# Optimization experiments

Measured on AMD Instinct MI355X. Metric: run time of the kernel, lower is better.

## Reference

```python
import jax, jax.numpy as jnp
import numpy as np

D = 512      # d_encoder
H = 8        # num_attn_heads
DH = 64      # d_attn
B = 8
S = 1024


def setup_inputs() -> dict:
    key = jax.random.key(0)
    ks = jax.random.split(key, 12)
    lim_in = 1.0 / np.sqrt(D)
    inp = {
        "Q": jax.random.normal(ks[0], (B, S, D), dtype=jnp.float32),
        "K": jax.random.normal(ks[1], (B, S, D), dtype=jnp.float32),
        "V": jax.random.normal(ks[2], (B, S, D), dtype=jnp.float32),
        # per-head projection weights stacked over heads: [H, D, DH]
        "Wq": jax.random.uniform(ks[3], (H, D, DH), jnp.float32, -lim_in, lim_in),
        "bq": jax.random.uniform(ks[4], (H, DH), jnp.float32, -lim_in, lim_in),
        "Wk": jax.random.uniform(ks[5], (H, D, DH), jnp.float32, -lim_in, lim_in),
        "bk": jax.random.uniform(ks[6], (H, DH), jnp.float32, -lim_in, lim_in),
        "Wv": jax.random.uniform(ks[7], (H, D, DH), jnp.float32, -lim_in, lim_in),
        "bv": jax.random.uniform(ks[8], (H, DH), jnp.float32, -lim_in, lim_in),
        "Wo": jax.random.uniform(ks[9], (D, D), jnp.float32, -lim_in, lim_in),
        "bo": jax.random.uniform(ks[10], (D,), jnp.float32, -lim_in, lim_in),
    }
    return inp


def reference(Q, K, V, Wq, bq, Wk, bk, Wv, bv, Wo, bo):
    scale = 1.0 / np.sqrt(DH).astype(np.float32)
    # per-head projections (the torch loop over heads, batched): [B,H,S,DH]
    Qh = jnp.einsum("bsd,hde->bhse", Q, Wq) + bq[None, :, None, :]
    Kh = jnp.einsum("bsd,hde->bhse", K, Wk) + bk[None, :, None, :]
    Vh = jnp.einsum("bsd,hde->bhse", V, Wv) + bv[None, :, None, :]
    # scaled dot-product attention with materialized scores [B,H,S,S]
    scores = jnp.einsum("bhse,bhte->bhst", Qh, Kh) * scale
    probs = jax.nn.softmax(scores, axis=-1)
    x = jnp.einsum("bhst,bhte->bhse", probs, Vh)  # [B,H,S,DH]
    # NOTE: original torch code does x.view(B, S, H*DH) directly on the
    # (B,H,S,DH) contiguous tensor WITHOUT transposing heads/time; we
    # faithfully replicate that memory-layout reshape.
    x = x.reshape(B, S, H * DH)
    x = x @ Wo + bo
    # dropout p=0.0 (p_drop set to 0 for deterministic reference)
    return x
```

## Files before the change

### kernel.cpp

```cpp
#include <hip/hip_runtime.h>
#include <hip/hip_bf16.h>

#define D_ENC 512
#define NH 8
#define DHD 64
#define BB 8
#define SS 1024

typedef unsigned short u16;
typedef __attribute__((ext_vector_type(8))) short short8;
typedef __attribute__((ext_vector_type(4))) float floatx4;

#define QSCALE 0.18033688011112042f

__device__ inline u16 f2bf(float f) {
    __hip_bfloat16 h = __float2bfloat16(f);
    return *reinterpret_cast<u16*>(&h);
}

__device__ inline void glds16(const u16* g, u16* l) {
    __builtin_amdgcn_global_load_lds(
        (const __attribute__((address_space(1))) void*)g,
        (__attribute__((address_space(3))) void*)l, 16, 0, 0);
}

__global__ __launch_bounds__(256) void prep_all(
    const float* __restrict__ Wq, const float* __restrict__ Wk,
    const float* __restrict__ Wv, const float* __restrict__ Wo,
    const float* __restrict__ Q, const float* __restrict__ K,
    const float* __restrict__ V,
    u16* __restrict__ WqT, u16* __restrict__ WkT, u16* __restrict__ WvT,
    u16* __restrict__ WoT, u16* __restrict__ Xbf)
{
    int bx = blockIdx.x;
    if (bx < 4096) {
        int tid = bx * 256 + threadIdx.x;
        const int WSZ = NH * D_ENC * DHD;
        if (tid < 3 * WSZ) {
            int wi = tid / WSZ, r = tid % WSZ;
            int d = r & 511;
            int e = (r >> 9) & 63;
            int h = r >> 15;
            const float* src = wi == 0 ? Wq : (wi == 1 ? Wk : Wv);
            u16* dst = wi == 0 ? WqT : (wi == 1 ? WkT : WvT);
            dst[r] = f2bf(src[h * (D_ENC * DHD) + d * DHD + e]);
        } else {
            int r = tid - 3 * WSZ;
            int d = r & 511, n = r >> 9;
            WoT[r] = f2bf(Wo[d * D_ENC + n]);
        }
    } else {
        int t = (bx - 4096) * 256 + threadIdx.x;
        int p = t / 524288, i = t % 524288;
        const float* src = p == 0 ? Q : (p == 1 ? K : V);
        const float4* s4 = reinterpret_cast<const float4*>(src) + (size_t)i * 2;
        float4 a = s4[0], b = s4[1];
        u16 hv[8] = { f2bf(a.x), f2bf(a.y), f2bf(a.z), f2bf(a.w),
                      f2bf(b.x), f2bf(b.y), f2bf(b.z), f2bf(b.w) };
        *reinterpret_cast<uint4*>(Xbf + (size_t)t * 8) =
            *reinterpret_cast<const uint4*>(hv);
    }
}

__global__ __launch_bounds__(256, 3) void qkv_gemm(
    const u16* __restrict__ Xbf,
    const u16* __restrict__ WqT, const u16* __restrict__ WkT,
    const u16* __restrict__ WvT,
    const float* __restrict__ bq, const float* __restrict__ bk,
    const float* __restrict__ bv,
    u16* __restrict__ Qh, u16* __restrict__ Kh, u16* __restrict__ VhT)
{
    const int proj = blockIdx.z;
    const u16* X = Xbf + (size_t)proj * (BB * SS * D_ENC);
    const u16* WT = proj == 0 ? WqT : (proj == 1 ? WkT : WvT);
    const float* bias = proj == 0 ? bq : (proj == 1 ? bk : bv);
    u16* out = proj == 0 ? Qh : (proj == 1 ? Kh : VhT);
    const float oscale = proj == 0 ? QSCALE : 1.0f;

    const int m0 = blockIdx.x * 128;
    const int n0 = blockIdx.y * 64;
    __shared__ __align__(16) u16 smem[24576];

    const int tid = threadIdx.x, lane = tid & 63, w = tid >> 6;
    const int q = lane >> 4, l15 = lane & 15;
    const int lr = lane >> 3;
    const int lc = (lane & 7) ^ (lr & 7);

    floatx4 acc[2][4] = {};

    #pragma unroll
    for (int j = 0; j < 4; ++j) {
        int r = (j * 4 + w) * 8 + lr;
        glds16(X + (size_t)(m0 + r) * D_ENC + lc * 8, smem + (j * 4 + w) * 512);
    }
    #pragma unroll
    for (int j = 0; j < 2; ++j) {
        int r = (j * 4 + w) * 8 + lr;
        glds16(WT + (size_t)(n0 + r) * D_ENC + lc * 8,
               smem + 16384 + (j * 4 + w) * 512);
    }

    for (int t = 0; t < 8; ++t) {
        __syncthreads();
        if (t + 1 < 8) {
            const int d1 = (t + 1) * 64;
            u16* ad = smem + ((t + 1) & 1) * 8192;
            u16* bd = smem + 16384 + ((t + 1) & 1) * 4096;
            #pragma unroll
            for (int j = 0; j < 4; ++j) {
                int r = (j * 4 + w) * 8 + lr;
                glds16(X + (size_t)(m0 + r) * D_ENC + d1 + lc * 8,
                       ad + (j * 4 + w) * 512);
            }
            #pragma unroll
            for (int j = 0; j < 2; ++j) {
                int r = (j * 4 + w) * 8 + lr;
                glds16(WT + (size_t)(n0 + r) * D_ENC + d1 + lc * 8,
                       bd + (j * 4 + w) * 512);
            }
        }
        const u16* as_ = smem + (t & 1) * 8192;
        const u16* bs_ = smem + 16384 + (t & 1) * 4096;
        #pragma unroll
        for (int ks = 0; ks < 2; ++ks) {
            const int co = ((ks * 4 + q) ^ (l15 & 7)) * 8;
            short8 a0 = *(const short8*)&as_[(32 * w + l15) * 64 + co];
            short8 a1 = *(const short8*)&as_[(32 * w + 16 + l15) * 64 + co];
            #pragma unroll
            for (int f = 0; f < 4; ++f) {
                short8 bf = *(const short8*)&bs_[(f * 16 + l15) * 64 + co];
                acc[0][f] = __builtin_amdgcn_mfma_f32_16x16x32_bf16(a0, bf, acc[0][f], 0, 0, 0);
                acc[1][f] = __builtin_amdgcn_mfma_f32_16x16x32_bf16(a1, bf, acc[1][f], 0, 0, 0);
            }
        }
    }

    const int b = m0 >> 10, sb = m0 & 1023, h = n0 >> 6;
    if (proj < 2) {
        u16* dst = out + ((size_t)(b * NH + h) * SS + sb) * DHD;
        #pragma unroll
        for (int i = 0; i < 2; ++i)
            #pragma unroll
            for (int f = 0; f < 4; ++f) {
                float bv_ = bias[n0 + f * 16 + l15];
                #pragma unroll
                for (int r = 0; r < 4; ++r)
                    dst[(32 * w + 16 * i + q * 4 + r) * DHD + f * 16 + l15] =
                        f2bf((acc[i][f][r] + bv_) * oscale);
            }
    } else {
        __syncthreads();
        #pragma unroll
        for (int i = 0; i < 2; ++i)
            #pragma unroll
            for (int f = 0; f < 4; ++f) {
                float bv_ = bias[n0 + f * 16 + l15];
                #pragma unroll
                for (int r = 0; r < 4; ++r)
                    smem[(f * 16 + l15) * 136 + 32 * w + 16 * i + q * 4 + r] =
                        f2bf(acc[i][f][r] + bv_);
            }
        __syncthreads();
        u16* dst = out + (size_t)(b * NH + h) * DHD * SS + sb;
        #pragma unroll
        for (int p2 = 0; p2 < 4; ++p2) {
            int c = (tid + 256 * p2) * 8;
            int e = c >> 7, s = c & 127;
            uint4 v = *(const uint4*)&smem[e * 136 + s];
            *(uint4*)&dst[(size_t)e * SS + s] = v;
        }
    }
}

__global__ __launch_bounds__(256, 4) void flash_attn(
    const u16* __restrict__ Qh, const u16* __restrict__ Kh,
    const u16* __restrict__ VhT, u16* __restrict__ Xb)
{
    const int i = blockIdx.x;
    const int s0 = (i >> 6) * 64;
    const size_t bh = (size_t)(((i >> 3) & 7) * 8 + (i & 7));

    __shared__ __align__(16) u16 Ks[2][64 * 64], Vs[2][64 * 64], Ps[64 * 64];

    const int tid = threadIdx.x, lane = tid & 63, w = tid >> 6;
    const int q = lane >> 4, l15 = lane & 15;
    const int lr = lane >> 3, lc = (lane & 7) ^ (lr & 7);

    const u16* qrow = Qh + (bh * SS + s0 + 16 * w + l15) * DHD;
    short8 qb0 = *(const short8*)(qrow + q * 8);
    short8 qb1 = *(const short8*)(qrow + 32 + q * 8);

    const u16* kbase = Kh + bh * SS * DHD;
    const u16* vbase = VhT + bh * DHD * SS;

    #pragma unroll
    for (int j = 0; j < 2; ++j) {
        int r = (j * 4 + w) * 8 + lr;
        glds16(kbase + (size_t)r * DHD + lc * 8, Ks[0] + (j * 4 + w) * 512);
        glds16(vbase + (size_t)r * SS + lc * 8, Vs[0] + (j * 4 + w) * 512);
    }

    floatx4 O[4] = {};
    floatx4 L = {0.f, 0.f, 0.f, 0.f};
    const short8 ones = {16256, 16256, 16256, 16256,
                         16256, 16256, 16256, 16256};

    for (int kt = 0; kt < SS / 64; ++kt) {
        __syncthreads();
        if (kt + 1 < SS / 64) {
            const int k1 = (kt + 1) * 64;
            u16* kd = Ks[(kt + 1) & 1];
            u16* vd = Vs[(kt + 1) & 1];
            #pragma unroll
            for (int j = 0; j < 2; ++j) {
                int r = (j * 4 + w) * 8 + lr;
                glds16(kbase + (size_t)(k1 + r) * DHD + lc * 8,
                       kd + (j * 4 + w) * 512);
                glds16(vbase + (size_t)r * SS + k1 + lc * 8,
                       vd + (j * 4 + w) * 512);
            }
        }
        const u16* ks_ = Ks[kt & 1];
        const u16* vs_ = Vs[kt & 1];

        floatx4 sacc[4] = {};
        #pragma unroll
        for (int f = 0; f < 4; ++f) {
            const int co0 = (q ^ (l15 & 7)) * 8;
            const int co1 = ((4 + q) ^ (l15 & 7)) * 8;
            short8 ka0 = *(const short8*)&ks_[(f * 16 + l15) * 64 + co0];
            short8 ka1 = *(const short8*)&ks_[(f * 16 + l15) * 64 + co1];
            sacc[f] = __builtin_amdgcn_mfma_f32_16x16x32_bf16(ka0, qb0, sacc[f], 0, 0, 0);
            sacc[f] = __builtin_amdgcn_mfma_f32_16x16x32_bf16(ka1, qb1, sacc[f], 0, 0, 0);
        }

        #pragma unroll
        for (int f = 0; f < 4; ++f) {
            ushort4 pk;
            pk.x = f2bf(__builtin_amdgcn_exp2f(sacc[f][0]));
            pk.y = f2bf(__builtin_amdgcn_exp2f(sacc[f][1]));
            pk.z = f2bf(__builtin_amdgcn_exp2f(sacc[f][2]));
            pk.w = f2bf(__builtin_amdgcn_exp2f(sacc[f][3]));
            const int chunk = (2 * f + (q >> 1)) ^ (l15 & 7);
            *(ushort4*)&Ps[(16 * w + l15) * 64 + chunk * 8 + (q & 1) * 4] = pk;
        }

        #pragma unroll
        for (int ks = 0; ks < 2; ++ks) {
            const int co = ((ks * 4 + q) ^ (l15 & 7)) * 8;
            short8 pa = *(const short8*)&Ps[(16 * w + l15) * 64 + co];
            L = __builtin_amdgcn_mfma_f32_16x16x32_bf16(pa, ones, L, 0, 0, 0);
            #pragma unroll
            for (int f = 0; f < 4; ++f) {
                short8 vb = *(const short8*)&vs_[(f * 16 + l15) * 64 + co];
                O[f] = __builtin_amdgcn_mfma_f32_16x16x32_bf16(pa, vb, O[f], 0, 0, 0);
            }
        }
    }

    u16* dst = Xb + (bh * SS + s0) * DHD;
    #pragma unroll
    for (int f = 0; f < 4; ++f)
        #pragma unroll
        for (int r = 0; r < 4; ++r)
            dst[(16 * w + q * 4 + r) * DHD + f * 16 + l15] =
                f2bf(O[f][r] / L[r]);
}

__global__ __launch_bounds__(256, 3) void out_gemm(
    const u16* __restrict__ X, const u16* __restrict__ WT,
    const float* __restrict__ bias, float* __restrict__ out)
{
    const int m0 = blockIdx.x * 128;
    const int n0 = blockIdx.y * 64;
    __shared__ __align__(16) u16 smem[24576];

    const int tid = threadIdx.x, lane = tid & 63, w = tid >> 6;
    const int q = lane >> 4, l15 = lane & 15;
    const int lr = lane >> 3, lc = (lane & 7) ^ (lr & 7);

    floatx4 acc[2][4] = {};

    #pragma unroll
    for (int j = 0; j < 4; ++j) {
        int r = (j * 4 + w) * 8 + lr;
        glds16(X + (size_t)(m0 + r) * D_ENC + lc * 8, smem + (j * 4 + w) * 512);
    }
    #pragma unroll
    for (int j = 0; j < 2; ++j) {
        int r = (j * 4 + w) * 8 + lr;
        glds16(WT + (size_t)(n0 + r) * D_ENC + lc * 8,
               smem + 16384 + (j * 4 + w) * 512);
    }

    for (int t = 0; t < 8; ++t) {
        __syncthreads();
        if (t + 1 < 8) {
            const int d1 = (t + 1) * 64;
            u16* ad = smem + ((t + 1) & 1) * 8192;
            u16* bd = smem + 16384 + ((t + 1) & 1) * 4096;
            #pragma unroll
            for (int j = 0; j < 4; ++j) {
                int r = (j * 4 + w) * 8 + lr;
                glds16(X + (size_t)(m0 + r) * D_ENC + d1 + lc * 8,
                       ad + (j * 4 + w) * 512);
            }
            #pragma unroll
            for (int j = 0; j < 2; ++j) {
                int r = (j * 4 + w) * 8 + lr;
                glds16(WT + (size_t)(n0 + r) * D_ENC + d1 + lc * 8,
                       bd + (j * 4 + w) * 512);
            }
        }
        const u16* as_ = smem + (t & 1) * 8192;
        const u16* bs_ = smem + 16384 + (t & 1) * 4096;
        #pragma unroll
        for (int ks = 0; ks < 2; ++ks) {
            const int co = ((ks * 4 + q) ^ (l15 & 7)) * 8;
            short8 a0 = *(const short8*)&as_[(32 * w + l15) * 64 + co];
            short8 a1 = *(const short8*)&as_[(32 * w + 16 + l15) * 64 + co];
            #pragma unroll
            for (int f = 0; f < 4; ++f) {
                short8 bf = *(const short8*)&bs_[(f * 16 + l15) * 64 + co];
                acc[0][f] = __builtin_amdgcn_mfma_f32_16x16x32_bf16(a0, bf, acc[0][f], 0, 0, 0);
                acc[1][f] = __builtin_amdgcn_mfma_f32_16x16x32_bf16(a1, bf, acc[1][f], 0, 0, 0);
            }
        }
    }
    #pragma unroll
    for (int i = 0; i < 2; ++i)
        #pragma unroll
        for (int f = 0; f < 4; ++f) {
            float bv_ = bias[n0 + f * 16 + l15];
            #pragma unroll
            for (int r = 0; r < 4; ++r)
                out[(size_t)(m0 + 32 * w + 16 * i + q * 4 + r) * D_ENC +
                    n0 + f * 16 + l15] = acc[i][f][r] + bv_;
        }
}

extern "C" void kernel_launch(void* const* d_in, const int* in_sizes, int n_in,
                              void* d_out, int out_size, void* d_ws, size_t ws_size,
                              hipStream_t stream)
{
    const float* Q  = (const float*)d_in[0];
    const float* K  = (const float*)d_in[1];
    const float* V  = (const float*)d_in[2];
    const float* Wq = (const float*)d_in[3];
    const float* bq = (const float*)d_in[4];
    const float* Wk = (const float*)d_in[5];
    const float* bk = (const float*)d_in[6];
    const float* Wv = (const float*)d_in[7];
    const float* bv = (const float*)d_in[8];
    const float* Wo = (const float*)d_in[9];
    const float* bo = (const float*)d_in[10];
    float* out = (float*)d_out;

    char* ws = (char*)d_ws;
    u16* WqT = (u16*)(ws + 0);
    u16* WkT = (u16*)(ws + 524288);
    u16* WvT = (u16*)(ws + 1048576);
    u16* WoT = (u16*)(ws + 1572864);
    u16* Xbf = (u16*)(ws + 2097152);
    u16* Xb  = (u16*)(ws + 2097152);
    u16* Qh  = (u16*)(ws + 27262976);
    u16* Kh  = (u16*)(ws + 35651584);
    u16* VhT = (u16*)(ws + 44040192);

    hipLaunchKernelGGL(prep_all, dim3(10240), dim3(256), 0, stream,
                       Wq, Wk, Wv, Wo, Q, K, V, WqT, WkT, WvT, WoT, Xbf);
    hipLaunchKernelGGL(qkv_gemm, dim3(64, 8, 3), dim3(256), 0, stream,
                       Xbf, WqT, WkT, WvT, bq, bk, bv, Qh, Kh, VhT);
    hipLaunchKernelGGL(flash_attn, dim3(1024), dim3(256), 0, stream,
                       Qh, Kh, VhT, Xb);
    hipLaunchKernelGGL(out_gemm, dim3(64, 8), dim3(256), 0, stream,
                       Xb, WoT, bo, out);
}
```

Baseline: 165.2 us.

## Fuse fp32-to-bf16 input conversion into QKV GEMM A-tile loading

Removes the separate conversion of Q/K/V to bf16 from the prep kernel and has the QKV GEMM load fp32 activations into registers, convert them, and store bf16 into swizzled LDS, prefetching the next tile during MFMA work. This eliminates a full write and re-read of a bf16 activation copy. The trade-off is that each GEMM block now reads fp32 A repeatedly across N-tiles, and the kernel gains register pressure and loses the async global-to-LDS path for A.

```diff
diff --git a/kernel.cpp b/kernel.cpp
--- a/kernel.cpp
+++ b/kernel.cpp
@@ -24,46 +24,32 @@
         (__attribute__((address_space(3))) void*)l, 16, 0, 0);
 }
 
-__global__ __launch_bounds__(256) void prep_all(
+__global__ __launch_bounds__(256) void prep_w(
     const float* __restrict__ Wq, const float* __restrict__ Wk,
     const float* __restrict__ Wv, const float* __restrict__ Wo,
-    const float* __restrict__ Q, const float* __restrict__ K,
-    const float* __restrict__ V,
     u16* __restrict__ WqT, u16* __restrict__ WkT, u16* __restrict__ WvT,
-    u16* __restrict__ WoT, u16* __restrict__ Xbf)
-{
-    int bx = blockIdx.x;
-    if (bx < 4096) {
-        int tid = bx * 256 + threadIdx.x;
-        const int WSZ = NH * D_ENC * DHD;
-        if (tid < 3 * WSZ) {
-            int wi = tid / WSZ, r = tid % WSZ;
-            int d = r & 511;
-            int e = (r >> 9) & 63;
-            int h = r >> 15;
-            const float* src = wi == 0 ? Wq : (wi == 1 ? Wk : Wv);
-            u16* dst = wi == 0 ? WqT : (wi == 1 ? WkT : WvT);
-            dst[r] = f2bf(src[h * (D_ENC * DHD) + d * DHD + e]);
-        } else {
-            int r = tid - 3 * WSZ;
-            int d = r & 511, n = r >> 9;
-            WoT[r] = f2bf(Wo[d * D_ENC + n]);
-        }
+    u16* __restrict__ WoT)
+{
+    int tid = blockIdx.x * 256 + threadIdx.x;
+    const int WSZ = NH * D_ENC * DHD;
+    if (tid < 3 * WSZ) {
+        int wi = tid / WSZ, r = tid % WSZ;
+        int d = r & 511;
+        int e = (r >> 9) & 63;
+        int h = r >> 15;
+        const float* src = wi == 0 ? Wq : (wi == 1 ? Wk : Wv);
+        u16* dst = wi == 0 ? WqT : (wi == 1 ? WkT : WvT);
+        dst[r] = f2bf(src[h * (D_ENC * DHD) + d * DHD + e]);
     } else {
-        int t = (bx - 4096) * 256 + threadIdx.x;
-        int p = t / 524288, i = t % 524288;
-        const float* src = p == 0 ? Q : (p == 1 ? K : V);
-        const float4* s4 = reinterpret_cast<const float4*>(src) + (size_t)i * 2;
-        float4 a = s4[0], b = s4[1];
-        u16 hv[8] = { f2bf(a.x), f2bf(a.y), f2bf(a.z), f2bf(a.w),
-                      f2bf(b.x), f2bf(b.y), f2bf(b.z), f2bf(b.w) };
-        *reinterpret_cast<uint4*>(Xbf + (size_t)t * 8) =
-            *reinterpret_cast<const uint4*>(hv);
+        int r = tid - 3 * WSZ;
+        int d = r & 511, n = r >> 9;
+        WoT[r] = f2bf(Wo[d * D_ENC + n]);
     }
 }
 
 __global__ __launch_bounds__(256, 3) void qkv_gemm(
-    const u16* __restrict__ Xbf,
+    const float* __restrict__ Qi, const float* __restrict__ Ki,
+    const float* __restrict__ Vi,
     const u16* __restrict__ WqT, const u16* __restrict__ WkT,
     const u16* __restrict__ WvT,
     const float* __restrict__ bq, const float* __restrict__ bk,
@@ -71,7 +57,7 @@
     u16* __restrict__ Qh, u16* __restrict__ Kh, u16* __restrict__ VhT)
 {
     const int proj = blockIdx.z;
-    const u16* X = Xbf + (size_t)proj * (BB * SS * D_ENC);
+    const float* X = proj == 0 ? Qi : (proj == 1 ? Ki : Vi);
     const u16* WT = proj == 0 ? WqT : (proj == 1 ? WkT : WvT);
     const float* bias = proj == 0 ? bq : (proj == 1 ? bk : bv);
     u16* out = proj == 0 ? Qh : (proj == 1 ? Kh : VhT);
@@ -87,11 +73,13 @@
     const int lc = (lane & 7) ^ (lr & 7);
 
     floatx4 acc[2][4] = {};
+    float4 av[4][2];
 
     #pragma unroll
     for (int j = 0; j < 4; ++j) {
         int r = (j * 4 + w) * 8 + lr;
-        glds16(X + (size_t)(m0 + r) * D_ENC + lc * 8, smem + (j * 4 + w) * 512);
+        const float4* src = (const float4*)&X[(size_t)(m0 + r) * D_ENC + lc * 8];
+        av[j][0] = src[0]; av[j][1] = src[1];
     }
     #pragma unroll
     for (int j = 0; j < 2; ++j) {
@@ -99,19 +87,29 @@
         glds16(WT + (size_t)(n0 + r) * D_ENC + lc * 8,
                smem + 16384 + (j * 4 + w) * 512);
     }
+    #pragma unroll
+    for (int j = 0; j < 4; ++j) {
+        int r = (j * 4 + w) * 8 + lr;
+        u16 hv[8] = { f2bf(av[j][0].x), f2bf(av[j][0].y),
+                      f2bf(av[j][0].z), f2bf(av[j][0].w),
+                      f2bf(av[j][1].x), f2bf(av[j][1].y),
+                      f2bf(av[j][1].z), f2bf(av[j][1].w) };
+        *(uint4*)&smem[r * 64 + (lane & 7) * 8] =
+            *reinterpret_cast<const uint4*>(hv);
+    }
 
     for (int t = 0; t < 8; ++t) {
         __syncthreads();
         if (t + 1 < 8) {
             const int d1 = (t + 1) * 64;
-            u16* ad = smem + ((t + 1) & 1) * 8192;
+            #pragma unroll
+            for (int j = 0; j < 4; ++j) {
+                int r = (j * 4 + w) * 8 + lr;
+                const float4* src =
+                    (const float4*)&X[(size_t)(m0 + r) * D_ENC + d1 + lc * 8];
+                av[j][0] = src[0]; av[j][1] = src[1];
+            }
             u16* bd = smem + 16384 + ((t + 1) & 1) * 4096;
-            #pragma unroll
-            for (int j = 0; j < 4; ++j) {
-                int r = (j * 4 + w) * 8 + lr;
-                glds16(X + (size_t)(m0 + r) * D_ENC + d1 + lc * 8,
-                       ad + (j * 4 + w) * 512);
-            }
             #pragma unroll
             for (int j = 0; j < 2; ++j) {
                 int r = (j * 4 + w) * 8 + lr;
@@ -131,6 +129,19 @@
                 short8 bf = *(const short8*)&bs_[(f * 16 + l15) * 64 + co];
                 acc[0][f] = __builtin_amdgcn_mfma_f32_16x16x32_bf16(a0, bf, acc[0][f], 0, 0, 0);
                 acc[1][f] = __builtin_amdgcn_mfma_f32_16x16x32_bf16(a1, bf, acc[1][f], 0, 0, 0);
+            }
+        }
+        if (t + 1 < 8) {
+            u16* ad = smem + ((t + 1) & 1) * 8192;
+            #pragma unroll
+            for (int j = 0; j < 4; ++j) {
+                int r = (j * 4 + w) * 8 + lr;
+                u16 hv[8] = { f2bf(av[j][0].x), f2bf(av[j][0].y),
+                              f2bf(av[j][0].z), f2bf(av[j][0].w),
+                              f2bf(av[j][1].x), f2bf(av[j][1].y),
+                              f2bf(av[j][1].z), f2bf(av[j][1].w) };
+                *(uint4*)&ad[r * 64 + (lane & 7) * 8] =
+                    *reinterpret_cast<const uint4*>(hv);
             }
         }
     }
@@ -361,16 +372,15 @@
     u16* WkT = (u16*)(ws + 524288);
     u16* WvT = (u16*)(ws + 1048576);
     u16* WoT = (u16*)(ws + 1572864);
-    u16* Xbf = (u16*)(ws + 2097152);
-    u16* Xb  = (u16*)(ws + 2097152);
-    u16* Qh  = (u16*)(ws + 27262976);
-    u16* Kh  = (u16*)(ws + 35651584);
-    u16* VhT = (u16*)(ws + 44040192);
-
-    hipLaunchKernelGGL(prep_all, dim3(10240), dim3(256), 0, stream,
-                       Wq, Wk, Wv, Wo, Q, K, V, WqT, WkT, WvT, WoT, Xbf);
+    u16* Qh  = (u16*)(ws + 2097152);
+    u16* Kh  = (u16*)(ws + 10485760);
+    u16* VhT = (u16*)(ws + 18874368);
+    u16* Xb  = (u16*)(ws + 27262976);
+
+    hipLaunchKernelGGL(prep_w, dim3(4096), dim3(256), 0, stream,
+                       Wq, Wk, Wv, Wo, WqT, WkT, WvT, WoT);
     hipLaunchKernelGGL(qkv_gemm, dim3(64, 8, 3), dim3(256), 0, stream,
-                       Xbf, WqT, WkT, WvT, bq, bk, bv, Qh, Kh, VhT);
+                       Q, K, V, WqT, WkT, WvT, bq, bk, bv, Qh, Kh, VhT);
     hipLaunchKernelGGL(flash_attn, dim3(1024), dim3(256), 0, stream,
                        Qh, Kh, VhT, Xb);
     hipLaunchKernelGGL(out_gemm, dim3(64, 8), dim3(256), 0, stream,
```

Measured after the change: 173.8 us. +5.2%, slower.
